# Kernel tuning notes

Measured on AMD Instinct MI355X. Metric: run time of the kernel, lower is better.

The kernel has to match this reference:

```python
import jax, jax.numpy as jnp
import numpy as np

WIN = 7
HEADS = 6
DIM = 192

def _relative_position_index(ws):
    coords = np.stack(np.meshgrid(np.arange(ws[0]), np.arange(ws[1]), indexing='ij'))  # (2, Wh, Ww)
    flat = coords.reshape(2, -1)  # (2, N)
    rel = flat[:, :, None] - flat[:, None, :]  # (2, N, N)
    rel = rel.transpose(1, 2, 0).copy()
    rel[:, :, 0] += ws[0] - 1
    rel[:, :, 1] += ws[1] - 1
    idx = rel[:, :, 0] * (2 * ws[1] - 1) + rel[:, :, 1]
    return idx.astype(np.int32)  # (N, N)

def setup_inputs() -> dict:
    key = jax.random.key(0)
    ks = jax.random.split(key, 6)
    B_, N, C = 4096, WIN * WIN, DIM
    x = jax.random.normal(ks[0], (B_, N, C), dtype=jnp.float32)
    qkv_w = jax.random.normal(ks[1], (3 * C, C), dtype=jnp.float32) * 0.02
    qkv_b = jax.random.normal(ks[2], (3 * C,), dtype=jnp.float32) * 0.02
    proj_w = jax.random.normal(ks[3], (C, C), dtype=jnp.float32) * 0.02
    proj_b = jax.random.normal(ks[4], (C,), dtype=jnp.float32) * 0.02
    bias_table = jax.random.normal(ks[5], ((2 * WIN - 1) ** 2, HEADS), dtype=jnp.float32) * 0.02
    rel_idx = jnp.asarray(_relative_position_index((WIN, WIN)))  # (N, N) int32
    return {"x": x, "qkv_w": qkv_w, "qkv_b": qkv_b, "proj_w": proj_w,
            "proj_b": proj_b, "bias_table": bias_table, "rel_idx": rel_idx}

def reference(x, qkv_w, qkv_b, proj_w, proj_b, bias_table, rel_idx):
    B_, N, C = x.shape
    H = HEADS
    Dh = C // H
    scale = Dh ** -0.5
    # qkv: (B_, N, 3C) -> (3, B_, H, N, Dh)
    qkv = (x @ qkv_w.T + qkv_b).reshape(B_, N, 3, H, Dh).transpose(2, 0, 3, 1, 4)
    q, k, v = qkv[0], qkv[1], qkv[2]
    attn = jnp.einsum('bhnd,bhmd->bhnm', q, k) * scale  # (B_, H, N, N)
    bias = bias_table[rel_idx]  # (N, N, H)
    attn = attn + bias.transpose(2, 0, 1)[None]  # (1, H, N, N) broadcast
    attn = jax.nn.softmax(attn, axis=-1)
    out = jnp.einsum('bhnm,bhmd->bhnd', attn, v)  # (B_, H, N, Dh)
    out = out.transpose(0, 2, 1, 3).reshape(B_, N, C)
    return out @ proj_w.T + proj_b
```

## Files before the change

kernel.cpp:

```cpp
#include <hip/hip_runtime.h>
#include <hip/hip_bf16.h>

#define NTOK 49
#define HEADS 6
#define DIM 192
#define DH 32

typedef short s8v __attribute__((ext_vector_type(8)));
typedef float f4v __attribute__((ext_vector_type(4)));

#define MFMA16(a, b, c) __builtin_amdgcn_mfma_f32_16x16x32_bf16((a), (b), (c), 0, 0, 0)

__device__ inline short f2bf(float f) {
    __hip_bfloat16 h = __float2bfloat16(f);
    return __builtin_bit_cast(short, h);
}

__device__ inline s8v ld_bf8(const float* __restrict__ p) {
    float4 f0 = *(const float4*)p;
    float4 f1 = *(const float4*)(p + 4);
    s8v r;
    r[0] = f2bf(f0.x); r[1] = f2bf(f0.y); r[2] = f2bf(f0.z); r[3] = f2bf(f0.w);
    r[4] = f2bf(f1.x); r[5] = f2bf(f1.y); r[6] = f2bf(f1.z); r[7] = f2bf(f1.w);
    return r;
}

__global__ void prep_kernel(const float* __restrict__ qkv_w,
                            const float* __restrict__ proj_w,
                            const float* __restrict__ bias_table,
                            const int* __restrict__ rel_idx,
                            short* __restrict__ wq, short* __restrict__ wp,
                            float* __restrict__ biasM) {
    int tid = blockIdx.x * blockDim.x + threadIdx.x;
    int stride = gridDim.x * blockDim.x;
    for (int i = tid; i < 3 * DIM * DIM; i += stride) wq[i] = f2bf(qkv_w[i]);
    for (int i = tid; i < DIM * DIM; i += stride)     wp[i] = f2bf(proj_w[i]);
    for (int i = tid; i < HEADS * NTOK * NTOK; i += stride) {
        int h = i / (NTOK * NTOK), rc = i - h * (NTOK * NTOK);
        biasM[i] = bias_table[rel_idx[rc] * HEADS + h];
    }
}

__global__ __launch_bounds__(512) void fused3(
    const float* __restrict__ x, const short* __restrict__ wq,
    const float* __restrict__ qkv_b, const short* __restrict__ wp,
    const float* __restrict__ proj_b, const float* __restrict__ biasM,
    float* __restrict__ out)
{
    extern __shared__ __align__(16) short smem[];
    short* xs = smem;
    short* qs = smem + 12800;
    short* ks = smem + 25600;
    short* vs = smem + 38400;
    short* ps = smem + 52224;

    const int tid = threadIdx.x, w = tid >> 6, lane = tid & 63;
    const int quad = lane >> 4, l16 = lane & 15, b = blockIdx.x;

    {
        const float4* src = (const float4*)(x + (size_t)b * NTOK * DIM);
        for (int idx = tid; idx < 2352; idx += 512) {
            int n = idx / 48, c = idx % 48;
            float4 f = src[idx];
            short* dst = &xs[n * 200 + c * 4];
            dst[0] = f2bf(f.x); dst[1] = f2bf(f.y);
            dst[2] = f2bf(f.z); dst[3] = f2bf(f.w);
        }
        int* xz = (int*)xs;
        for (int i = tid; i < 1500; i += 512) xz[4900 + i] = 0;
    }
    __syncthreads();

    for (int nt = w; nt < 36; nt += 8) {
        const short* wrow = wq + (nt * 16 + l16) * DIM + quad * 8;
        s8v bw[6];
#pragma unroll
        for (int kb = 0; kb < 6; ++kb)
            bw[kb] = *(const s8v*)(wrow + kb * 32);

        f4v acc[4];
#pragma unroll
        for (int mt = 0; mt < 4; ++mt) acc[mt] = (f4v){0.f, 0.f, 0.f, 0.f};

#pragma unroll
        for (int kb = 0; kb < 6; ++kb) {
#pragma unroll
            for (int mt = 0; mt < 4; ++mt) {
                s8v a = *(const s8v*)&xs[(mt * 16 + l16) * 200 + kb * 32 + quad * 8];
                acc[mt] = MFMA16(a, bw[kb], acc[mt]);
            }
        }

        int t = nt / 12, hh = (nt % 12) >> 1, dh16 = (nt & 1) * 16;
        float bias = qkv_b[nt * 16 + l16];
        if (t == 2) {
            short* dst = &vs[(hh * DH + dh16 + l16) * 72];
#pragma unroll
            for (int mt = 0; mt < 4; ++mt)
#pragma unroll
                for (int r = 0; r < 4; ++r) {
                    int row = mt * 16 + quad * 4 + r;
                    dst[row] = f2bf(acc[mt][r] + bias);
                }
        } else {
            float scale = (t == 0) ? 0.17677669529663689f : 1.0f;
            short* dst = (t == 0 ? qs : ks) + hh * DH + dh16 + l16;
#pragma unroll
            for (int mt = 0; mt < 4; ++mt)
#pragma unroll
                for (int r = 0; r < 4; ++r) {
                    int row = mt * 16 + quad * 4 + r;
                    dst[row * 200] = f2bf((acc[mt][r] + bias) * scale);
                }
        }
    }
    __syncthreads();

    if (w < HEADS) {
        const int h = w;
        short* psw = ps + w * 4608;

        s8v aq[4], bk[4];
#pragma unroll
        for (int i = 0; i < 4; ++i)
            aq[i] = *(const s8v*)&qs[(i * 16 + l16) * 200 + h * DH + quad * 8];
#pragma unroll
        for (int i = 0; i < 4; ++i)
            bk[i] = *(const s8v*)&ks[(i * 16 + l16) * 200 + h * DH + quad * 8];

        f4v sacc[4][4];
#pragma unroll
        for (int mt = 0; mt < 4; ++mt)
#pragma unroll
            for (int nt = 0; nt < 4; ++nt)
                sacc[mt][nt] = MFMA16(aq[mt], bk[nt], ((f4v){0.f, 0.f, 0.f, 0.f}));

        const float* bmh = biasM + h * (NTOK * NTOK);
#pragma unroll
        for (int mt = 0; mt < 4; ++mt)
            for (int r = 0; r < 4; ++r) {
                int row = mt * 16 + quad * 4 + r;
                float sv[4];
#pragma unroll
                for (int nt = 0; nt < 4; ++nt) {
                    int col = nt * 16 + l16;
                    float s = sacc[mt][nt][r];
                    if (col < NTOK) {
                        if (row < NTOK) s += bmh[row * NTOK + col];
                    } else s = -30000.f;
                    sv[nt] = s;
                }
                float m = fmaxf(fmaxf(sv[0], sv[1]), fmaxf(sv[2], sv[3]));
                for (int d = 1; d < 16; d <<= 1) m = fmaxf(m, __shfl_xor(m, d));
                float p[4], sum = 0.f;
#pragma unroll
                for (int nt = 0; nt < 4; ++nt) {
                    p[nt] = exp2f((sv[nt] - m) * 1.4426950408889634f);
                    sum += p[nt];
                }
                for (int d = 1; d < 16; d <<= 1) sum += __shfl_xor(sum, d);
                float inv = 1.f / sum;
#pragma unroll
                for (int nt = 0; nt < 4; ++nt)
                    psw[row * 72 + nt * 16 + l16] = f2bf(p[nt] * inv);
            }

        f4v oacc[4][2];
#pragma unroll
        for (int mt = 0; mt < 4; ++mt)
#pragma unroll
            for (int nv = 0; nv < 2; ++nv) oacc[mt][nv] = (f4v){0.f, 0.f, 0.f, 0.f};
#pragma unroll
        for (int ks2 = 0; ks2 < 2; ++ks2) {
            s8v bv[2];
#pragma unroll
            for (int nv = 0; nv < 2; ++nv)
                bv[nv] = *(const s8v*)&vs[(h * DH + nv * 16 + l16) * 72 + ks2 * 32 + quad * 8];
#pragma unroll
            for (int mt = 0; mt < 4; ++mt) {
                s8v ap = *(const s8v*)&psw[(mt * 16 + l16) * 72 + ks2 * 32 + quad * 8];
#pragma unroll
                for (int nv = 0; nv < 2; ++nv)
                    oacc[mt][nv] = MFMA16(ap, bv[nv], oacc[mt][nv]);
            }
        }

        short* os = xs;
#pragma unroll
        for (int mt = 0; mt < 4; ++mt)
#pragma unroll
            for (int nv = 0; nv < 2; ++nv)
#pragma unroll
                for (int r = 0; r < 4; ++r) {
                    int row = mt * 16 + quad * 4 + r;
                    os[row * 200 + h * DH + nv * 16 + l16] = f2bf(oacc[mt][nv][r]);
                }
    }
    __syncthreads();

    for (int nt = w; nt < 12; nt += 8) {
        const short* wrow = wp + (nt * 16 + l16) * DIM + quad * 8;
        s8v bw[6];
#pragma unroll
        for (int kb = 0; kb < 6; ++kb)
            bw[kb] = *(const s8v*)(wrow + kb * 32);

        f4v acc[4];
#pragma unroll
        for (int mt = 0; mt < 4; ++mt) acc[mt] = (f4v){0.f, 0.f, 0.f, 0.f};

#pragma unroll
        for (int kb = 0; kb < 6; ++kb) {
#pragma unroll
            for (int mt = 0; mt < 4; ++mt) {
                s8v a = *(const s8v*)&xs[(mt * 16 + l16) * 200 + kb * 32 + quad * 8];
                acc[mt] = MFMA16(a, bw[kb], acc[mt]);
            }
        }

        int j0 = nt * 16 + l16;
        float bias = proj_b[j0];
        float* dst = out + (size_t)b * NTOK * DIM + j0;
#pragma unroll
        for (int mt = 0; mt < 4; ++mt)
#pragma unroll
            for (int r = 0; r < 4; ++r) {
                int row = mt * 16 + quad * 4 + r;
                if (row < NTOK) dst[row * DIM] = acc[mt][r] + bias;
            }
    }
}

__global__ __launch_bounds__(512) void qkv_kernel(
    const float* __restrict__ x, const short* __restrict__ wq,
    const float* __restrict__ qkv_b,
    short* __restrict__ q_ws, short* __restrict__ k_ws, short* __restrict__ v_ws)
{
    __shared__ __align__(16) short xs[64 * 200];
    __shared__ __align__(16) short vbuf[192 * 72];

    const int tid = threadIdx.x, w = tid >> 6, lane = tid & 63;
    const int quad = lane >> 4, l16 = lane & 15, b = blockIdx.x;

    {
        const float4* src = (const float4*)(x + (size_t)b * NTOK * DIM);
        for (int idx = tid; idx < 2352; idx += 512) {
            int n = idx / 48, c = idx % 48;
            float4 f = src[idx];
            short* dst = &xs[n * 200 + c * 4];
            dst[0] = f2bf(f.x); dst[1] = f2bf(f.y);
            dst[2] = f2bf(f.z); dst[3] = f2bf(f.w);
        }
        int* xz = (int*)xs;
        for (int i = tid; i < 1500; i += 512) xz[4900 + i] = 0;
        for (int i = tid; i < 192 * 23; i += 512) {
            int row = i / 23, t = 49 + i % 23;
            vbuf[row * 72 + t] = 0;
        }
    }
    __syncthreads();

    for (int nt = w; nt < 36; nt += 8) {
        const short* wrow = wq + (nt * 16 + l16) * DIM + quad * 8;
        s8v bw[6];
#pragma unroll
        for (int kb = 0; kb < 6; ++kb) bw[kb] = *(const s8v*)(wrow + kb * 32);
        f4v acc[4];
#pragma unroll
        for (int mt = 0; mt < 4; ++mt) acc[mt] = (f4v){0.f, 0.f, 0.f, 0.f};
#pragma unroll
        for (int kb = 0; kb < 6; ++kb)
#pragma unroll
            for (int mt = 0; mt < 4; ++mt) {
                s8v a = *(const s8v*)&xs[(mt * 16 + l16) * 200 + kb * 32 + quad * 8];
                acc[mt] = MFMA16(a, bw[kb], acc[mt]);
            }
        int t = nt / 12, hh = (nt % 12) >> 1, dh16 = (nt & 1) * 16;
        float bias = qkv_b[nt * 16 + l16];
        if (t == 2) {
            short* dst = &vbuf[(hh * DH + dh16 + l16) * 72];
#pragma unroll
            for (int mt = 0; mt < 4; ++mt)
#pragma unroll
                for (int r = 0; r < 4; ++r) {
                    int row = mt * 16 + quad * 4 + r;
                    if (row < NTOK) dst[row] = f2bf(acc[mt][r] + bias);
                }
        } else {
            float scale = (t == 0) ? 0.17677669529663689f : 1.0f;
            short* dst = (t == 0 ? q_ws : k_ws)
                       + (size_t)(b * HEADS + hh) * NTOK * DH + dh16 + l16;
#pragma unroll
            for (int mt = 0; mt < 4; ++mt)
#pragma unroll
                for (int r = 0; r < 4; ++r) {
                    int row = mt * 16 + quad * 4 + r;
                    if (row < NTOK) dst[row * DH] = f2bf((acc[mt][r] + bias) * scale);
                }
        }
    }
    __syncthreads();

    {
        short* dstbase = v_ws + (size_t)b * 192 * 64;
        for (int c = tid; c < 1536; c += 512) {
            int row = c >> 3, tk = (c & 7) * 8;
            *(int4*)(dstbase + row * 64 + tk) = *(const int4*)&vbuf[row * 72 + tk];
        }
    }
}

__global__ __launch_bounds__(384) void attn_kernel(
    const short* __restrict__ k_ws, const short* __restrict__ v_ws,
    const float* __restrict__ biasM, short* qo_ws)
{
    __shared__ __align__(16) short ps[6 * 64 * 72];

    const int tid = threadIdx.x, w = tid >> 6, lane = tid & 63;
    const int quad = lane >> 4, l16 = lane & 15, b = blockIdx.x;
    const int h = w;
    short* psw = ps + w * 4608;

    const short* qb = qo_ws + (size_t)(b * HEADS + h) * NTOK * DH;
    const short* kb = k_ws  + (size_t)(b * HEADS + h) * NTOK * DH;
    const short* vb = v_ws  + (size_t)(b * HEADS + h) * DH * 64;

    s8v aq[4], bk[4];
    for (int i = 0; i < 4; ++i)
        aq[i] = *(const s8v*)(qb + (i * 16 + l16) * DH + quad * 8);
    for (int i = 0; i < 4; ++i)
        bk[i] = *(const s8v*)(kb + (i * 16 + l16) * DH + quad * 8);

    f4v sacc[4][4];
    for (int mt = 0; mt < 4; ++mt)
        for (int nt = 0; nt < 4; ++nt)
            sacc[mt][nt] = MFMA16(aq[mt], bk[nt], ((f4v){0.f, 0.f, 0.f, 0.f}));

    const float* bmh = biasM + h * (NTOK * NTOK);
    for (int mt = 0; mt < 4; ++mt)
        for (int r = 0; r < 4; ++r) {
            int row = mt * 16 + quad * 4 + r;
            float sv[4];
            for (int nt = 0; nt < 4; ++nt) {
                int col = nt * 16 + l16;
                float s = sacc[mt][nt][r];
                if (col < NTOK) {
                    if (row < NTOK) s += bmh[row * NTOK + col];
                } else s = -30000.f;
                sv[nt] = s;
            }
            float m = fmaxf(fmaxf(sv[0], sv[1]), fmaxf(sv[2], sv[3]));
            for (int d = 1; d < 16; d <<= 1) m = fmaxf(m, __shfl_xor(m, d));
            float p[4], sum = 0.f;
            for (int nt = 0; nt < 4; ++nt) {
                p[nt] = exp2f((sv[nt] - m) * 1.4426950408889634f);
                sum += p[nt];
            }
            for (int d = 1; d < 16; d <<= 1) sum += __shfl_xor(sum, d);
            float inv = 1.f / sum;
            for (int nt = 0; nt < 4; ++nt)
                psw[row * 72 + nt * 16 + l16] = f2bf(p[nt] * inv);
        }

    f4v oacc[4][2];
    for (int mt = 0; mt < 4; ++mt)
        for (int nv = 0; nv < 2; ++nv) oacc[mt][nv] = (f4v){0.f, 0.f, 0.f, 0.f};
    for (int ks = 0; ks < 2; ++ks) {
        s8v bv[2];
        for (int nv = 0; nv < 2; ++nv)
            bv[nv] = *(const s8v*)(vb + (nv * 16 + l16) * 64 + ks * 32 + quad * 8);
        for (int mt = 0; mt < 4; ++mt) {
            s8v ap = *(const s8v*)&psw[(mt * 16 + l16) * 72 + ks * 32 + quad * 8];
            for (int nv = 0; nv < 2; ++nv)
                oacc[mt][nv] = MFMA16(ap, bv[nv], oacc[mt][nv]);
        }
    }

    __syncthreads();

    for (int mt = 0; mt < 4; ++mt)
        for (int nv = 0; nv < 2; ++nv)
            for (int r = 0; r < 4; ++r) {
                int row = mt * 16 + quad * 4 + r;
                if (row < NTOK)
                    qo_ws[((size_t)(b * NTOK + row) * HEADS + h) * DH + nv * 16 + l16] =
                        f2bf(oacc[mt][nv][r]);
            }
}

__global__ __launch_bounds__(256) void proj_kernel(
    const short* __restrict__ o_ws, const short* __restrict__ wp,
    const float* __restrict__ proj_b, float* __restrict__ out)
{
    __shared__ __align__(16) short os[64 * 200];
    const int tid = threadIdx.x, w = tid >> 6, lane = tid & 63;
    const int quad = lane >> 4, l16 = lane & 15, b = blockIdx.x;

    {
        const short* src = o_ws + (size_t)b * NTOK * DIM;
        for (int c = tid; c < 1176; c += 256) {
            int n = c / 24, cc = (c % 24) * 8;
            *(int4*)&os[n * 200 + cc] = *(const int4*)(src + n * DIM + cc);
        }
        int* oz = (int*)os;
        for (int i = tid; i < 1500; i += 256) oz[4900 + i] = 0;
    }
    __syncthreads();

    for (int nt = w; nt < 12; nt += 4) {
        const short* wrow = wp + (nt * 16 + l16) * DIM + quad * 8;
        s8v bw[6];
#pragma unroll
        for (int kb = 0; kb < 6; ++kb) bw[kb] = *(const s8v*)(wrow + kb * 32);
        f4v acc[4];
#pragma unroll
        for (int mt = 0; mt < 4; ++mt) acc[mt] = (f4v){0.f, 0.f, 0.f, 0.f};
#pragma unroll
        for (int kb = 0; kb < 6; ++kb)
#pragma unroll
            for (int mt = 0; mt < 4; ++mt) {
                s8v a = *(const s8v*)&os[(mt * 16 + l16) * 200 + kb * 32 + quad * 8];
                acc[mt] = MFMA16(a, bw[kb], acc[mt]);
            }
        int j0 = nt * 16 + l16;
        float bias = proj_b[j0];
        float* dst = out + (size_t)b * NTOK * DIM + j0;
#pragma unroll
        for (int mt = 0; mt < 4; ++mt)
#pragma unroll
            for (int r = 0; r < 4; ++r) {
                int row = mt * 16 + quad * 4 + r;
                if (row < NTOK) dst[row * DIM] = acc[mt][r] + bias;
            }
    }
}

__global__ __launch_bounds__(512) void winattn_fused(
    const float* __restrict__ x, const float* __restrict__ qkv_w,
    const float* __restrict__ qkv_b, const float* __restrict__ proj_w,
    const float* __restrict__ proj_b, const float* __restrict__ bias_table,
    const int* __restrict__ rel_idx, float* __restrict__ out)
{
    __shared__ __align__(16) short xs[64 * 200];
    __shared__ __align__(16) short qs[64 * 40];
    __shared__ __align__(16) short ks[64 * 40];
    __shared__ __align__(16) short vs[32 * 72];
    __shared__ __align__(16) short pp[64 * 72];

    const int tid = threadIdx.x, w = tid >> 6, lane = tid & 63;
    const int quad = lane >> 4, l16 = lane & 15, b = blockIdx.x;
    const int mt = w & 3, half = w >> 2;

    {
        const float4* src = (const float4*)(x + (size_t)b * NTOK * DIM);
        for (int idx = tid; idx < 2352; idx += 512) {
            int n = idx / 48, c = idx % 48;
            float4 f = src[idx];
            short* dst = &xs[n * 200 + c * 4];
            dst[0] = f2bf(f.x); dst[1] = f2bf(f.y);
            dst[2] = f2bf(f.z); dst[3] = f2bf(f.w);
        }
        int* xz = (int*)xs;
        for (int i = tid; i < 1500; i += 512) xz[4900 + i] = 0;
    }
    __syncthreads();

    f4v acc_p[6];
    for (int i = 0; i < 6; i++) acc_p[i] = (f4v){0.f, 0.f, 0.f, 0.f};

    for (int h = 0; h < HEADS; ++h) {
        {
            f4v acc[3];
            for (int i = 0; i < 3; i++) acc[i] = (f4v){0.f, 0.f, 0.f, 0.f};
            int jbase[3];
            for (int i = 0; i < 3; i++) {
                int tn = half * 3 + i;
                int t = tn >> 1, dpart = (tn & 1) * 16;
                jbase[i] = t * DIM + h * DH + dpart + l16;
            }
            for (int kb2 = 0; kb2 < 6; ++kb2) {
                s8v a = *(const s8v*)&xs[(mt * 16 + l16) * 200 + kb2 * 32 + quad * 8];
                for (int i = 0; i < 3; i++) {
                    s8v bf = ld_bf8(qkv_w + jbase[i] * DIM + kb2 * 32 + quad * 8);
                    acc[i] = MFMA16(a, bf, acc[i]);
                }
            }
            for (int i = 0; i < 3; i++) {
                int tn = half * 3 + i;
                int t = tn >> 1, dpart = (tn & 1) * 16;
                float bias = qkv_b[jbase[i]];
                for (int r = 0; r < 4; r++) {
                    int row = mt * 16 + quad * 4 + r;
                    float v = acc[i][r] + bias;
                    if (t == 0)      qs[row * 40 + dpart + l16] = f2bf(v * 0.17677669529663689f);
                    else if (t == 1) ks[row * 40 + dpart + l16] = f2bf(v);
                    else             vs[(dpart + l16) * 72 + row] = f2bf(v);
                }
            }
        }
        __syncthreads();
        if (w < 4) {
            f4v sacc[4];
            for (int i = 0; i < 4; i++) sacc[i] = (f4v){0.f, 0.f, 0.f, 0.f};
            s8v a = *(const s8v*)&qs[(w * 16 + l16) * 40 + quad * 8];
            for (int nt = 0; nt < 4; nt++) {
                s8v bf = *(const s8v*)&ks[(nt * 16 + l16) * 40 + quad * 8];
                sacc[nt] = MFMA16(a, bf, sacc[nt]);
            }
            for (int r = 0; r < 4; r++) {
                int row = w * 16 + quad * 4 + r;
                float sv[4];
                for (int nt = 0; nt < 4; nt++) {
                    int col = nt * 16 + l16;
                    float s = sacc[nt][r];
                    if (col < NTOK) {
                        if (row < NTOK)
                            s += bias_table[rel_idx[row * NTOK + col] * HEADS + h];
                    } else s = -30000.f;
                    sv[nt] = s;
                }
                float m = fmaxf(fmaxf(sv[0], sv[1]), fmaxf(sv[2], sv[3]));
                for (int d = 1; d < 16; d <<= 1) m = fmaxf(m, __shfl_xor(m, d));
                float p[4], sum = 0.f;
                for (int nt = 0; nt < 4; nt++) {
                    p[nt] = exp2f((sv[nt] - m) * 1.4426950408889634f);
                    sum += p[nt];
                }
                for (int d = 1; d < 16; d <<= 1) sum += __shfl_xor(sum, d);
                float inv = 1.f / sum;
                for (int nt = 0; nt < 4; nt++)
                    pp[row * 72 + nt * 16 + l16] = f2bf(p[nt] * inv);
            }
        }
        __syncthreads();
        {
            f4v oacc = (f4v){0.f, 0.f, 0.f, 0.f};
            for (int kb2 = 0; kb2 < 2; kb2++) {
                s8v a  = *(const s8v*)&pp[(mt * 16 + l16) * 72 + kb2 * 32 + quad * 8];
                s8v bf = *(const s8v*)&vs[(half * 16 + l16) * 72 + kb2 * 32 + quad * 8];
                oacc = MFMA16(a, bf, oacc);
            }
            for (int r = 0; r < 4; r++) {
                int row = mt * 16 + quad * 4 + r;
                qs[row * 40 + half * 16 + l16] = f2bf(oacc[r]);
            }
        }
        __syncthreads();
        {
            s8v a = *(const s8v*)&qs[(mt * 16 + l16) * 40 + quad * 8];
            for (int i = 0; i < 6; i++) {
                int ncol = half * 96 + i * 16 + l16;
                s8v bf = ld_bf8(proj_w + ncol * DIM + h * DH + quad * 8);
                acc_p[i] = MFMA16(a, bf, acc_p[i]);
            }
        }
        __syncthreads();
    }
    for (int i = 0; i < 6; i++) {
        int ncol = half * 96 + i * 16 + l16;
        float bias = proj_b[ncol];
        for (int r = 0; r < 4; r++) {
            int row = mt * 16 + quad * 4 + r;
            if (row < NTOK)
                out[((size_t)b * NTOK + row) * DIM + ncol] = acc_p[i][r] + bias;
        }
    }
}

extern "C" void kernel_launch(void* const* d_in, const int* in_sizes, int n_in,
                              void* d_out, int out_size, void* d_ws, size_t ws_size,
                              hipStream_t stream) {
    const float* x          = (const float*)d_in[0];
    const float* qkv_w      = (const float*)d_in[1];
    const float* qkv_b      = (const float*)d_in[2];
    const float* proj_w     = (const float*)d_in[3];
    const float* proj_b     = (const float*)d_in[4];
    const float* bias_table = (const float*)d_in[5];
    const int*   rel_idx    = (const int*)d_in[6];
    float*       out        = (float*)d_out;

    const int B_ = in_sizes[0] / (NTOK * DIM);

    const size_t FUSED_LDS = 159744;
    static int smem_ok = -1;
    if (smem_ok < 0) {
        smem_ok = (hipFuncSetAttribute((const void*)fused3,
                       hipFuncAttributeMaxDynamicSharedMemorySize,
                       (int)FUSED_LDS) == hipSuccess) ? 1 : 0;
    }

    const size_t sz_wq = (size_t)3 * DIM * DIM * 2;
    const size_t sz_wp = (size_t)DIM * DIM * 2;
    const size_t sz_bm = (size_t)HEADS * NTOK * NTOK * 4;
    const size_t need_fused = sz_wq + sz_wp + sz_bm;

    const size_t sz_q  = (size_t)B_ * HEADS * NTOK * DH * 2;
    const size_t sz_k  = sz_q;
    const size_t sz_v  = (size_t)B_ * HEADS * DH * 64 * 2;
    const size_t need_split = sz_q + sz_k + sz_v + sz_wq + sz_wp + sz_bm;

    if (smem_ok == 1 && ws_size >= need_fused) {
        char* p = (char*)d_ws;
        short* wq    = (short*)p;  p += sz_wq;
        short* wp    = (short*)p;  p += sz_wp;
        float* biasM = (float*)p;

        prep_kernel<<<dim3(128), dim3(256), 0, stream>>>(
            qkv_w, proj_w, bias_table, rel_idx, wq, wp, biasM);
        fused3<<<dim3(B_), dim3(512), FUSED_LDS, stream>>>(
            x, wq, qkv_b, wp, proj_b, biasM, out);
    } else if (ws_size >= need_split) {
        char* p = (char*)d_ws;
        short* q_ws  = (short*)p;  p += sz_q;
        short* k_ws  = (short*)p;  p += sz_k;
        short* v_ws  = (short*)p;  p += sz_v;
        short* wq    = (short*)p;  p += sz_wq;
        short* wp    = (short*)p;  p += sz_wp;
        float* biasM = (float*)p;

        prep_kernel<<<dim3(128), dim3(256), 0, stream>>>(
            qkv_w, proj_w, bias_table, rel_idx, wq, wp, biasM);
        qkv_kernel<<<dim3(B_), dim3(512), 0, stream>>>(
            x, wq, qkv_b, q_ws, k_ws, v_ws);
        attn_kernel<<<dim3(B_), dim3(384), 0, stream>>>(
            k_ws, v_ws, biasM, q_ws);
        proj_kernel<<<dim3(B_), dim3(256), 0, stream>>>(
            q_ws, wp, proj_b, out);
    } else {
        winattn_fused<<<dim3(B_), dim3(512), 0, stream>>>(
            x, qkv_w, qkv_b, proj_w, proj_b, bias_table, rel_idx, out);
    }
}
```

Before: 575.1 us.

## Make fused kernel persistent with double-buffered prefetch of next window input

Converts the one-block-per-window fused kernel into a persistent kernel with a grid capped at 512 blocks, each looping over windows. The next window's x is loaded into registers during the QKV GEMM and written into a second LDS buffer during the output stage, so global load latency overlaps compute. LDS use drops by reusing the q region and the current x buffer for softmax probabilities. Q/K fragments are read into registers before a barrier so their LDS can be overwritten. The extra prefetch registers and the fixed grid size may reduce occupancy or leave CUs unevenly loaded.

Result: slower. 698.5 us (+21.5%).

```diff
diff --git a/kernel.cpp b/kernel.cpp
--- a/kernel.cpp
+++ b/kernel.cpp
@@ -41,193 +41,236 @@
     }
 }
 
-__global__ __launch_bounds__(512) void fused3(
+__global__ __launch_bounds__(512, 2) void fused4(
     const float* __restrict__ x, const short* __restrict__ wq,
     const float* __restrict__ qkv_b, const short* __restrict__ wp,
     const float* __restrict__ proj_b, const float* __restrict__ biasM,
-    float* __restrict__ out)
+    float* __restrict__ out, int B_)
 {
     extern __shared__ __align__(16) short smem[];
-    short* xs = smem;
-    short* qs = smem + 12800;
-    short* ks = smem + 25600;
-    short* vs = smem + 38400;
-    short* ps = smem + 52224;
+    short* xsA = smem;
+    short* xsB = smem + 12800;
+    short* qs  = smem + 25600;
+    short* ks  = smem + 38400;
+    short* vs  = smem + 51200;
 
     const int tid = threadIdx.x, w = tid >> 6, lane = tid & 63;
-    const int quad = lane >> 4, l16 = lane & 15, b = blockIdx.x;
+    const int quad = lane >> 4, l16 = lane & 15;
+    const int G = gridDim.x;
+
+    int win = blockIdx.x;
+
+    auto stage_write = [&](short* dst, int idx, float4 f) {
+        int n = idx / 48, c = idx % 48;
+        int lo = (f2bf(f.x) & 0xffff) | (((int)f2bf(f.y)) << 16);
+        int hi = (f2bf(f.z) & 0xffff) | (((int)f2bf(f.w)) << 16);
+        *(int2*)&dst[n * 200 + c * 4] = make_int2(lo, hi);
+    };
 
     {
-        const float4* src = (const float4*)(x + (size_t)b * NTOK * DIM);
-        for (int idx = tid; idx < 2352; idx += 512) {
-            int n = idx / 48, c = idx % 48;
-            float4 f = src[idx];
-            short* dst = &xs[n * 200 + c * 4];
-            dst[0] = f2bf(f.x); dst[1] = f2bf(f.y);
-            dst[2] = f2bf(f.z); dst[3] = f2bf(f.w);
-        }
-        int* xz = (int*)xs;
+        const float4* src = (const float4*)(x + (size_t)win * NTOK * DIM);
+        if (tid        < 2352) stage_write(xsA, tid,        src[tid]);
+        if (tid + 512  < 2352) stage_write(xsA, tid + 512,  src[tid + 512]);
+        if (tid + 1024 < 2352) stage_write(xsA, tid + 1024, src[tid + 1024]);
+        if (tid + 1536 < 2352) stage_write(xsA, tid + 1536, src[tid + 1536]);
+        if (tid + 2048 < 2352) stage_write(xsA, tid + 2048, src[tid + 2048]);
+        int* xz = (int*)xsA;
         for (int i = tid; i < 1500; i += 512) xz[4900 + i] = 0;
     }
     __syncthreads();
 
-    for (int nt = w; nt < 36; nt += 8) {
-        const short* wrow = wq + (nt * 16 + l16) * DIM + quad * 8;
-        s8v bw[6];
-#pragma unroll
-        for (int kb = 0; kb < 6; ++kb)
-            bw[kb] = *(const s8v*)(wrow + kb * 32);
-
-        f4v acc[4];
-#pragma unroll
-        for (int mt = 0; mt < 4; ++mt) acc[mt] = (f4v){0.f, 0.f, 0.f, 0.f};
-
-#pragma unroll
-        for (int kb = 0; kb < 6; ++kb) {
-#pragma unroll
-            for (int mt = 0; mt < 4; ++mt) {
-                s8v a = *(const s8v*)&xs[(mt * 16 + l16) * 200 + kb * 32 + quad * 8];
-                acc[mt] = MFMA16(a, bw[kb], acc[mt]);
-            }
-        }
-
-        int t = nt / 12, hh = (nt % 12) >> 1, dh16 = (nt & 1) * 16;
-        float bias = qkv_b[nt * 16 + l16];
-        if (t == 2) {
-            short* dst = &vs[(hh * DH + dh16 + l16) * 72];
+    int cur = 0;
+    for (;;) {
+        short* xs = cur ? xsB : xsA;
+        short* xn = cur ? xsA : xsB;
+        const int nwin = win + G;
+        const bool has_next = (nwin < B_);
+
+        float4 pf0, pf1, pf2, pf3, pf4;
+        if (has_next) {
+            const float4* src = (const float4*)(x + (size_t)nwin * NTOK * DIM);
+            if (tid        < 2352) pf0 = src[tid];
+            if (tid + 512  < 2352) pf1 = src[tid + 512];
+            if (tid + 1024 < 2352) pf2 = src[tid + 1024];
+            if (tid + 1536 < 2352) pf3 = src[tid + 1536];
+            if (tid + 2048 < 2352) pf4 = src[tid + 2048];
+        }
+
+        for (int nt = w; nt < 36; nt += 8) {
+            const short* wrow = wq + (nt * 16 + l16) * DIM + quad * 8;
+            s8v bw[6];
+#pragma unroll
+            for (int kb = 0; kb < 6; ++kb)
+                bw[kb] = *(const s8v*)(wrow + kb * 32);
+
+            f4v acc[4];
+#pragma unroll
+            for (int mt = 0; mt < 4; ++mt) acc[mt] = (f4v){0.f, 0.f, 0.f, 0.f};
+
+#pragma unroll
+            for (int kb = 0; kb < 6; ++kb) {
+#pragma unroll
+                for (int mt = 0; mt < 4; ++mt) {
+                    s8v a = *(const s8v*)&xs[(mt * 16 + l16) * 200 + kb * 32 + quad * 8];
+                    acc[mt] = MFMA16(a, bw[kb], acc[mt]);
+                }
+            }
+
+            int t = nt / 12, hh = (nt % 12) >> 1, dh16 = (nt & 1) * 16;
+            float bias = qkv_b[nt * 16 + l16];
+            if (t == 2) {
+                short* dst = &vs[(hh * DH + dh16 + l16) * 72];
+#pragma unroll
+                for (int mt = 0; mt < 4; ++mt)
+#pragma unroll
+                    for (int r = 0; r < 4; ++r) {
+                        int row = mt * 16 + quad * 4 + r;
+                        dst[row] = f2bf(acc[mt][r] + bias);
+                    }
+            } else {
+                float scale = (t == 0) ? 0.17677669529663689f : 1.0f;
+                short* dst = (t == 0 ? qs : ks) + hh * DH + dh16 + l16;
+#pragma unroll
+                for (int mt = 0; mt < 4; ++mt)
+#pragma unroll
+                    for (int r = 0; r < 4; ++r) {
+                        int row = mt * 16 + quad * 4 + r;
+                        dst[row * 200] = f2bf((acc[mt][r] + bias) * scale);
+                    }
+            }
+        }
+        __syncthreads();
+
+        s8v aq[4], bk[4];
+        if (w < HEADS) {
+#pragma unroll
+            for (int i = 0; i < 4; ++i)
+                aq[i] = *(const s8v*)&qs[(i * 16 + l16) * 200 + w * DH + quad * 8];
+#pragma unroll
+            for (int i = 0; i < 4; ++i)
+                bk[i] = *(const s8v*)&ks[(i * 16 + l16) * 200 + w * DH + quad * 8];
+        }
+        __syncthreads();
+
+        f4v oacc[4][2];
+        if (w < HEADS) {
+            const int h = w;
+            short* psw = (w == 5) ? xs : (qs + w * 4608);
+
+            f4v sacc[4][4];
 #pragma unroll
             for (int mt = 0; mt < 4; ++mt)
 #pragma unroll
+                for (int nt = 0; nt < 4; ++nt)
+                    sacc[mt][nt] = MFMA16(aq[mt], bk[nt], ((f4v){0.f, 0.f, 0.f, 0.f}));
+
+            const float* bmh = biasM + h * (NTOK * NTOK);
+#pragma unroll
+            for (int mt = 0; mt < 4; ++mt)
                 for (int r = 0; r < 4; ++r) {
                     int row = mt * 16 + quad * 4 + r;
-                    dst[row] = f2bf(acc[mt][r] + bias);
-                }
-        } else {
-            float scale = (t == 0) ? 0.17677669529663689f : 1.0f;
-            short* dst = (t == 0 ? qs : ks) + hh * DH + dh16 + l16;
+                    float sv[4];
+#pragma unroll
+                    for (int nt = 0; nt < 4; ++nt) {
+                        int col = nt * 16 + l16;
+                        float s = sacc[mt][nt][r];
+                        if (col < NTOK) {
+                            if (row < NTOK) s += bmh[row * NTOK + col];
+                        } else s = -30000.f;
+                        sv[nt] = s;
+                    }
+                    float m = fmaxf(fmaxf(sv[0], sv[1]), fmaxf(sv[2], sv[3]));
+                    for (int d = 1; d < 16; d <<= 1) m = fmaxf(m, __shfl_xor(m, d));
+                    float p[4], sum = 0.f;
+#pragma unroll
+                    for (int nt = 0; nt < 4; ++nt) {
+                        p[nt] = exp2f((sv[nt] - m) * 1.4426950408889634f);
+                        sum += p[nt];
+                    }
+                    for (int d = 1; d < 16; d <<= 1) sum += __shfl_xor(sum, d);
+                    float inv = 1.f / sum;
+#pragma unroll
+                    for (int nt = 0; nt < 4; ++nt)
+                        psw[row * 72 + nt * 16 + l16] = f2bf(p[nt] * inv);
+                }
+
+#pragma unroll
+            for (int mt = 0; mt < 4; ++mt)
+#pragma unroll
+                for (int nv = 0; nv < 2; ++nv) oacc[mt][nv] = (f4v){0.f, 0.f, 0.f, 0.f};
+#pragma unroll
+            for (int ks2 = 0; ks2 < 2; ++ks2) {
+                s8v bv[2];
+#pragma unroll
+                for (int nv = 0; nv < 2; ++nv)
+                    bv[nv] = *(const s8v*)&vs[(h * DH + nv * 16 + l16) * 72 + ks2 * 32 + quad * 8];
+#pragma unroll
+                for (int mt = 0; mt < 4; ++mt) {
+                    s8v ap = *(const s8v*)&psw[(mt * 16 + l16) * 72 + ks2 * 32 + quad * 8];
+#pragma unroll
+                    for (int nv = 0; nv < 2; ++nv)
+                        oacc[mt][nv] = MFMA16(ap, bv[nv], oacc[mt][nv]);
+                }
+            }
+        }
+        __syncthreads();
+
+        if (w < HEADS) {
+#pragma unroll
+            for (int mt = 0; mt < 4; ++mt)
+#pragma unroll
+                for (int nv = 0; nv < 2; ++nv)
+#pragma unroll
+                    for (int r = 0; r < 4; ++r) {
+                        int row = mt * 16 + quad * 4 + r;
+                        xs[row * 200 + w * DH + nv * 16 + l16] = f2bf(oacc[mt][nv][r]);
+                    }
+        }
+        if (has_next) {
+            if (tid        < 2352) stage_write(xn, tid,        pf0);
+            if (tid + 512  < 2352) stage_write(xn, tid + 512,  pf1);
+            if (tid + 1024 < 2352) stage_write(xn, tid + 1024, pf2);
+            if (tid + 1536 < 2352) stage_write(xn, tid + 1536, pf3);
+            if (tid + 2048 < 2352) stage_write(xn, tid + 2048, pf4);
+            int* xz = (int*)xn;
+            for (int i = tid; i < 1500; i += 512) xz[4900 + i] = 0;
+        }
+        __syncthreads();
+
+        for (int nt = w; nt < 12; nt += 8) {
+            const short* wrow = wp + (nt * 16 + l16) * DIM + quad * 8;
+            s8v bw[6];
+#pragma unroll
+            for (int kb = 0; kb < 6; ++kb)
+                bw[kb] = *(const s8v*)(wrow + kb * 32);
+
+            f4v acc[4];
+#pragma unroll
+            for (int mt = 0; mt < 4; ++mt) acc[mt] = (f4v){0.f, 0.f, 0.f, 0.f};
+
+#pragma unroll
+            for (int kb = 0; kb < 6; ++kb) {
+#pragma unroll
+                for (int mt = 0; mt < 4; ++mt) {
+                    s8v a = *(const s8v*)&xs[(mt * 16 + l16) * 200 + kb * 32 + quad * 8];
+                    acc[mt] = MFMA16(a, bw[kb], acc[mt]);
+                }
+            }
+
+            int j0 = nt * 16 + l16;
+            float bias = proj_b[j0];
+            float* dst = out + (size_t)win * NTOK * DIM + j0;
 #pragma unroll
             for (int mt = 0; mt < 4; ++mt)
 #pragma unroll
                 for (int r = 0; r < 4; ++r) {
                     int row = mt * 16 + quad * 4 + r;
-                    dst[row * 200] = f2bf((acc[mt][r] + bias) * scale);
-                }
-        }
-    }
-    __syncthreads();
-
-    if (w < HEADS) {
-        const int h = w;
-        short* psw = ps + w * 4608;
-
-        s8v aq[4], bk[4];
-#pragma unroll
-        for (int i = 0; i < 4; ++i)
-            aq[i] = *(const s8v*)&qs[(i * 16 + l16) * 200 + h * DH + quad * 8];
-#pragma unroll
-        for (int i = 0; i < 4; ++i)
-            bk[i] = *(const s8v*)&ks[(i * 16 + l16) * 200 + h * DH + quad * 8];
-
-        f4v sacc[4][4];
-#pragma unroll
-        for (int mt = 0; mt < 4; ++mt)
-#pragma unroll
-            for (int nt = 0; nt < 4; ++nt)
-                sacc[mt][nt] = MFMA16(aq[mt], bk[nt], ((f4v){0.f, 0.f, 0.f, 0.f}));
-
-        const float* bmh = biasM + h * (NTOK * NTOK);
-#pragma unroll
-        for (int mt = 0; mt < 4; ++mt)
-            for (int r = 0; r < 4; ++r) {
-                int row = mt * 16 + quad * 4 + r;
-                float sv[4];
-#pragma unroll
-                for (int nt = 0; nt < 4; ++nt) {
-                    int col = nt * 16 + l16;
-                    float s = sacc[mt][nt][r];
-                    if (col < NTOK) {
-                        if (row < NTOK) s += bmh[row * NTOK + col];
-                    } else s = -30000.f;
-                    sv[nt] = s;
-                }
-                float m = fmaxf(fmaxf(sv[0], sv[1]), fmaxf(sv[2], sv[3]));
-                for (int d = 1; d < 16; d <<= 1) m = fmaxf(m, __shfl_xor(m, d));
-                float p[4], sum = 0.f;
-#pragma unroll
-                for (int nt = 0; nt < 4; ++nt) {
-                    p[nt] = exp2f((sv[nt] - m) * 1.4426950408889634f);
-                    sum += p[nt];
-                }
-                for (int d = 1; d < 16; d <<= 1) sum += __shfl_xor(sum, d);
-                float inv = 1.f / sum;
-#pragma unroll
-                for (int nt = 0; nt < 4; ++nt)
-                    psw[row * 72 + nt * 16 + l16] = f2bf(p[nt] * inv);
-            }
-
-        f4v oacc[4][2];
-#pragma unroll
-        for (int mt = 0; mt < 4; ++mt)
-#pragma unroll
-            for (int nv = 0; nv < 2; ++nv) oacc[mt][nv] = (f4v){0.f, 0.f, 0.f, 0.f};
-#pragma unroll
-        for (int ks2 = 0; ks2 < 2; ++ks2) {
-            s8v bv[2];
-#pragma unroll
-            for (int nv = 0; nv < 2; ++nv)
-                bv[nv] = *(const s8v*)&vs[(h * DH + nv * 16 + l16) * 72 + ks2 * 32 + quad * 8];
-#pragma unroll
-            for (int mt = 0; mt < 4; ++mt) {
-                s8v ap = *(const s8v*)&psw[(mt * 16 + l16) * 72 + ks2 * 32 + quad * 8];
-#pragma unroll
-                for (int nv = 0; nv < 2; ++nv)
-                    oacc[mt][nv] = MFMA16(ap, bv[nv], oacc[mt][nv]);
-            }
-        }
-
-        short* os = xs;
-#pragma unroll
-        for (int mt = 0; mt < 4; ++mt)
-#pragma unroll
-            for (int nv = 0; nv < 2; ++nv)
-#pragma unroll
-                for (int r = 0; r < 4; ++r) {
-                    int row = mt * 16 + quad * 4 + r;
-                    os[row * 200 + h * DH + nv * 16 + l16] = f2bf(oacc[mt][nv][r]);
-                }
-    }
-    __syncthreads();
-
-    for (int nt = w; nt < 12; nt += 8) {
-        const short* wrow = wp + (nt * 16 + l16) * DIM + quad * 8;
-        s8v bw[6];
-#pragma unroll
-        for (int kb = 0; kb < 6; ++kb)
-            bw[kb] = *(const s8v*)(wrow + kb * 32);
-
-        f4v acc[4];
-#pragma unroll
-        for (int mt = 0; mt < 4; ++mt) acc[mt] = (f4v){0.f, 0.f, 0.f, 0.f};
-
-#pragma unroll
-        for (int kb = 0; kb < 6; ++kb) {
-#pragma unroll
-            for (int mt = 0; mt < 4; ++mt) {
-                s8v a = *(const s8v*)&xs[(mt * 16 + l16) * 200 + kb * 32 + quad * 8];
-                acc[mt] = MFMA16(a, bw[kb], acc[mt]);
-            }
-        }
-
-        int j0 = nt * 16 + l16;
-        float bias = proj_b[j0];
-        float* dst = out + (size_t)b * NTOK * DIM + j0;
-#pragma unroll
-        for (int mt = 0; mt < 4; ++mt)
-#pragma unroll
-            for (int r = 0; r < 4; ++r) {
-                int row = mt * 16 + quad * 4 + r;
-                if (row < NTOK) dst[row * DIM] = acc[mt][r] + bias;
-            }
+                    if (row < NTOK) dst[row * DIM] = acc[mt][r] + bias;
+                }
+        }
+
+        if (!has_next) break;
+        win = nwin; cur ^= 1;
     }
 }
 
@@ -581,10 +624,10 @@
 
     const int B_ = in_sizes[0] / (NTOK * DIM);
 
-    const size_t FUSED_LDS = 159744;
+    const size_t FUSED_LDS = 130048;
     static int smem_ok = -1;
     if (smem_ok < 0) {
-        smem_ok = (hipFuncSetAttribute((const void*)fused3,
+        smem_ok = (hipFuncSetAttribute((const void*)fused4,
                        hipFuncAttributeMaxDynamicSharedMemorySize,
                        (int)FUSED_LDS) == hipSuccess) ? 1 : 0;
     }
@@ -607,8 +650,9 @@
 
         prep_kernel<<<dim3(128), dim3(256), 0, stream>>>(
             qkv_w, proj_w, bias_table, rel_idx, wq, wp, biasM);
-        fused3<<<dim3(B_), dim3(512), FUSED_LDS, stream>>>(
-            x, wq, qkv_b, wp, proj_b, biasM, out);
+        int grid = B_ < 512 ? B_ : 512;
+        fused4<<<dim3(grid), dim3(512), FUSED_LDS, stream>>>(
+            x, wq, qkv_b, wp, proj_b, biasM, out, B_);
     } else if (ws_size >= need_split) {
         char* p = (char*)d_ws;
         short* q_ws  = (short*)p;  p += sz_q;
```

## Precompute bf16 x globally and shrink fused kernel LDS to raise occupancy

Applied to the files above, without the earlier changes.

Adds a separate pass that converts x to bf16 in workspace, and has the fused kernel read its QKV A-operands directly from global memory instead of staging x in LDS. The LDS buffers are then reused in place: Q/K fragments are loaded into registers, the probability tiles overwrite Q/K space with an XOR swizzle, and the attention output goes back into the Q buffer. This cuts LDS from about 156KB to 77KB so more blocks can be resident per CU. The cost is an extra global round trip for x in bf16, extra barriers, and uncached global A-loads repeated across waves.

After: 744.6 us. 1.29x slower.

```diff
diff --git a/kernel.cpp b/kernel.cpp
--- a/kernel.cpp
+++ b/kernel.cpp
@@ -10,6 +10,7 @@
 typedef float f4v __attribute__((ext_vector_type(4)));
 
 #define MFMA16(a, b, c) __builtin_amdgcn_mfma_f32_16x16x32_bf16((a), (b), (c), 0, 0, 0)
+#define PSWZ(row, off) ((((row) << 6) + (off)) ^ (((row) & 7) << 3))
 
 __device__ inline short f2bf(float f) {
     __hip_bfloat16 h = __float2bfloat16(f);
@@ -41,37 +42,32 @@
     }
 }
 
-__global__ __launch_bounds__(512) void fused3(
-    const float* __restrict__ x, const short* __restrict__ wq,
+__global__ __launch_bounds__(256) void prep_x(const float* __restrict__ x,
+                                              short* __restrict__ xbf, long n8) {
+    long i = (long)blockIdx.x * blockDim.x + threadIdx.x;
+    long stride = (long)gridDim.x * blockDim.x;
+    for (; i < n8; i += stride)
+        *(s8v*)(xbf + i * 8) = ld_bf8(x + i * 8);
+}
+
+__global__ __launch_bounds__(512, 4) void fused5(
+    const short* __restrict__ xbf, const short* __restrict__ wq,
     const float* __restrict__ qkv_b, const short* __restrict__ wp,
     const float* __restrict__ proj_b, const float* __restrict__ biasM,
     float* __restrict__ out)
 {
     extern __shared__ __align__(16) short smem[];
-    short* xs = smem;
-    short* qs = smem + 12800;
-    short* ks = smem + 25600;
-    short* vs = smem + 38400;
-    short* ps = smem + 52224;
+    short* qs = smem;
+    short* ks = smem + 12800;
+    short* vs = smem + 25600;
 
     const int tid = threadIdx.x, w = tid >> 6, lane = tid & 63;
     const int quad = lane >> 4, l16 = lane & 15, b = blockIdx.x;
 
-    {
-        const float4* src = (const float4*)(x + (size_t)b * NTOK * DIM);
-        for (int idx = tid; idx < 2352; idx += 512) {
-            int n = idx / 48, c = idx % 48;
-            float4 f = src[idx];
-            short* dst = &xs[n * 200 + c * 4];
-            dst[0] = f2bf(f.x); dst[1] = f2bf(f.y);
-            dst[2] = f2bf(f.z); dst[3] = f2bf(f.w);
-        }
-        int* xz = (int*)xs;
-        for (int i = tid; i < 1500; i += 512) xz[4900 + i] = 0;
-    }
-    __syncthreads();
+    const short* xw = xbf + (size_t)b * (NTOK * DIM);
 
     for (int nt = w; nt < 36; nt += 8) {
+        asm volatile("" ::: "memory");
         const short* wrow = wq + (nt * 16 + l16) * DIM + quad * 8;
         s8v bw[6];
 #pragma unroll
@@ -86,7 +82,9 @@
         for (int kb = 0; kb < 6; ++kb) {
 #pragma unroll
             for (int mt = 0; mt < 4; ++mt) {
-                s8v a = *(const s8v*)&xs[(mt * 16 + l16) * 200 + kb * 32 + quad * 8];
+                int row = mt * 16 + l16;
+                int crow = row < NTOK ? row : (NTOK - 1);
+                s8v a = *(const s8v*)(xw + crow * DIM + kb * 32 + quad * 8);
                 acc[mt] = MFMA16(a, bw[kb], acc[mt]);
             }
         }
@@ -116,17 +114,21 @@
     }
     __syncthreads();
 
+    s8v aq[4], bk[4];
+    if (w < HEADS) {
+#pragma unroll
+        for (int i = 0; i < 4; ++i)
+            aq[i] = *(const s8v*)&qs[(i * 16 + l16) * 200 + w * DH + quad * 8];
+#pragma unroll
+        for (int i = 0; i < 4; ++i)
+            bk[i] = *(const s8v*)&ks[(i * 16 + l16) * 200 + w * DH + quad * 8];
+    }
+    __syncthreads();
+
+    f4v oacc[4][2];
     if (w < HEADS) {
         const int h = w;
-        short* psw = ps + w * 4608;
-
-        s8v aq[4], bk[4];
-#pragma unroll
-        for (int i = 0; i < 4; ++i)
-            aq[i] = *(const s8v*)&qs[(i * 16 + l16) * 200 + h * DH + quad * 8];
-#pragma unroll
-        for (int i = 0; i < 4; ++i)
-            bk[i] = *(const s8v*)&ks[(i * 16 + l16) * 200 + h * DH + quad * 8];
+        short* psw = smem + w * 4096;
 
         f4v sacc[4][4];
 #pragma unroll
@@ -162,10 +164,9 @@
                 float inv = 1.f / sum;
 #pragma unroll
                 for (int nt = 0; nt < 4; ++nt)
-                    psw[row * 72 + nt * 16 + l16] = f2bf(p[nt] * inv);
-            }
-
-        f4v oacc[4][2];
+                    psw[PSWZ(row, nt * 16 + l16)] = f2bf(p[nt] * inv);
+            }
+
 #pragma unroll
         for (int mt = 0; mt < 4; ++mt)
 #pragma unroll
@@ -178,14 +179,16 @@
                 bv[nv] = *(const s8v*)&vs[(h * DH + nv * 16 + l16) * 72 + ks2 * 32 + quad * 8];
 #pragma unroll
             for (int mt = 0; mt < 4; ++mt) {
-                s8v ap = *(const s8v*)&psw[(mt * 16 + l16) * 72 + ks2 * 32 + quad * 8];
+                s8v ap = *(const s8v*)&psw[PSWZ(mt * 16 + l16, ks2 * 32 + quad * 8)];
 #pragma unroll
                 for (int nv = 0; nv < 2; ++nv)
                     oacc[mt][nv] = MFMA16(ap, bv[nv], oacc[mt][nv]);
             }
         }
-
-        short* os = xs;
+    }
+    __syncthreads();
+
+    if (w < HEADS) {
 #pragma unroll
         for (int mt = 0; mt < 4; ++mt)
 #pragma unroll
@@ -193,12 +196,13 @@
 #pragma unroll
                 for (int r = 0; r < 4; ++r) {
                     int row = mt * 16 + quad * 4 + r;
-                    os[row * 200 + h * DH + nv * 16 + l16] = f2bf(oacc[mt][nv][r]);
+                    qs[row * 200 + w * DH + nv * 16 + l16] = f2bf(oacc[mt][nv][r]);
                 }
     }
     __syncthreads();
 
     for (int nt = w; nt < 12; nt += 8) {
+        asm volatile("" ::: "memory");
         const short* wrow = wp + (nt * 16 + l16) * DIM + quad * 8;
         s8v bw[6];
 #pragma unroll
@@ -213,7 +217,7 @@
         for (int kb = 0; kb < 6; ++kb) {
 #pragma unroll
             for (int mt = 0; mt < 4; ++mt) {
-                s8v a = *(const s8v*)&xs[(mt * 16 + l16) * 200 + kb * 32 + quad * 8];
+                s8v a = *(const s8v*)&qs[(mt * 16 + l16) * 200 + kb * 32 + quad * 8];
                 acc[mt] = MFMA16(a, bw[kb], acc[mt]);
             }
         }
@@ -581,18 +585,19 @@
 
     const int B_ = in_sizes[0] / (NTOK * DIM);
 
-    const size_t FUSED_LDS = 159744;
+    const size_t FUSED_LDS = 78848;
     static int smem_ok = -1;
     if (smem_ok < 0) {
-        smem_ok = (hipFuncSetAttribute((const void*)fused3,
+        smem_ok = (hipFuncSetAttribute((const void*)fused5,
                        hipFuncAttributeMaxDynamicSharedMemorySize,
                        (int)FUSED_LDS) == hipSuccess) ? 1 : 0;
     }
 
-    const size_t sz_wq = (size_t)3 * DIM * DIM * 2;
-    const size_t sz_wp = (size_t)DIM * DIM * 2;
-    const size_t sz_bm = (size_t)HEADS * NTOK * NTOK * 4;
-    const size_t need_fused = sz_wq + sz_wp + sz_bm;
+    const size_t sz_xbf = (size_t)B_ * NTOK * DIM * 2;
+    const size_t sz_wq  = (size_t)3 * DIM * DIM * 2;
+    const size_t sz_wp  = (size_t)DIM * DIM * 2;
+    const size_t sz_bm  = (size_t)HEADS * NTOK * NTOK * 4;
+    const size_t need_fused = sz_xbf + sz_wq + sz_wp + sz_bm;
 
     const size_t sz_q  = (size_t)B_ * HEADS * NTOK * DH * 2;
     const size_t sz_k  = sz_q;
@@ -601,14 +606,17 @@
 
     if (smem_ok == 1 && ws_size >= need_fused) {
         char* p = (char*)d_ws;
+        short* xbf   = (short*)p;  p += sz_xbf;
         short* wq    = (short*)p;  p += sz_wq;
         short* wp    = (short*)p;  p += sz_wp;
         float* biasM = (float*)p;
 
+        long n8 = (long)B_ * NTOK * DIM / 8;
+        prep_x<<<dim3(2048), dim3(256), 0, stream>>>(x, xbf, n8);
         prep_kernel<<<dim3(128), dim3(256), 0, stream>>>(
             qkv_w, proj_w, bias_table, rel_idx, wq, wp, biasM);
-        fused3<<<dim3(B_), dim3(512), FUSED_LDS, stream>>>(
-            x, wq, qkv_b, wp, proj_b, biasM, out);
+        fused5<<<dim3(B_), dim3(512), FUSED_LDS, stream>>>(
+            xbf, wq, qkv_b, wp, proj_b, biasM, out);
     } else if (ws_size >= need_split) {
         char* p = (char*)d_ws;
         short* q_ws  = (short*)p;  p += sz_q;
```
